# Kernel tuning notes

Measured on AMD Instinct MI355X. Metric: run time of the kernel, lower is better.

Reference implementation:

```python
import jax, jax.numpy as jnp
import numpy as np

B, S, D, H = 4, 2048, 1024, 16
HD = D // H  # head dim = 64


def setup_inputs() -> dict:
    key = jax.random.key(0)
    ks = jax.random.split(key, 6)
    scale = D ** -0.5
    x = jax.random.normal(ks[0], (B, S, D), dtype=jnp.float32)
    # per-head q/k/v projections stacked: [H, D, HD] (bias-free, as in GPT Head)
    Wq = jax.random.normal(ks[1], (H, D, HD), dtype=jnp.float32) * scale
    Wk = jax.random.normal(ks[2], (H, D, HD), dtype=jnp.float32) * scale
    Wv = jax.random.normal(ks[3], (H, D, HD), dtype=jnp.float32) * scale
    # output projection Linear(D, D) with bias
    Wp = jax.random.normal(ks[4], (D, D), dtype=jnp.float32) * scale
    bp = jax.random.normal(ks[5], (D,), dtype=jnp.float32) * 0.01
    return {"x": x, "Wq": Wq, "Wk": Wk, "Wv": Wv, "Wp": Wp, "bp": bp}


def reference(x, Wq, Wk, Wv, Wp, bp):
    # q,k,v: [B, H, S, HD]
    q = jnp.einsum("bsd,hdk->bhsk", x, Wq)
    k = jnp.einsum("bsd,hdk->bhsk", x, Wk)
    v = jnp.einsum("bsd,hdk->bhsk", x, Wv)
    scale = HD ** -0.5
    # attention scores [B, H, S, S] with causal mask
    scores = jnp.einsum("bhsk,bhtk->bhst", q, k) * scale
    causal = jnp.tril(jnp.ones((S, S), dtype=bool))
    scores = jnp.where(causal, scores, jnp.finfo(scores.dtype).min)
    att = jax.nn.softmax(scores, axis=-1)
    out = jnp.einsum("bhst,bhtk->bhsk", att, v)  # [B, H, S, HD]
    # concat heads -> [B, S, D], then output projection
    out = out.transpose(0, 2, 1, 3).reshape(B, S, D)
    return out @ Wp + bp
```

## Files before the change

kernel.cpp:

```cpp
#include <hip/hip_runtime.h>
#include <stdint.h>

#define B_  4
#define S_  2048
#define D_  1024
#define H_  16
#define HD_ 64

typedef __attribute__((ext_vector_type(8))) short bf16x8;
typedef __attribute__((ext_vector_type(4))) short bf16x4;
typedef __attribute__((ext_vector_type(4))) float f32x4;

#define MFMA32(a, b, c) __builtin_amdgcn_mfma_f32_16x16x32_bf16(a, b, c, 0, 0, 0)

__device__ __forceinline__ unsigned short f2bf(float f) {
  union { float f; uint32_t u; } cv; cv.f = f;
  uint32_t x = cv.u;
  uint32_t r = (x + 0x7fffu + ((x >> 16) & 1u)) >> 16;
  return (unsigned short)r;
}

__device__ __forceinline__ unsigned short f2bf_rz(float f) {
  union { float f; uint32_t u; } cv; cv.f = f;
  return (unsigned short)(cv.u >> 16);
}

__device__ __forceinline__ float fexp2(float x) {
#if __has_builtin(__builtin_amdgcn_exp2f)
  return __builtin_amdgcn_exp2f(x);
#else
  return exp2f(x);
#endif
}

__device__ __forceinline__ void gload_lds16(const unsigned short* g, unsigned short* l) {
  __builtin_amdgcn_global_load_lds((const __attribute__((address_space(1))) void*)g,
                                   (__attribute__((address_space(3))) void*)l, 16, 0, 0);
}

__global__ void k_cast_x(const float* __restrict__ x, unsigned short* __restrict__ xb) {
  size_t i = ((size_t)blockIdx.x * 256 + threadIdx.x) * 8;
  float4 a = *(const float4*)(x + i);
  float4 b = *(const float4*)(x + i + 4);
  bf16x8 o;
  o[0] = (short)f2bf(a.x); o[1] = (short)f2bf(a.y);
  o[2] = (short)f2bf(a.z); o[3] = (short)f2bf(a.w);
  o[4] = (short)f2bf(b.x); o[5] = (short)f2bf(b.y);
  o[6] = (short)f2bf(b.z); o[7] = (short)f2bf(b.w);
  *(bf16x8*)(xb + i) = o;
}

__global__ void k_wqkv_t(const float* __restrict__ Wq, const float* __restrict__ Wk,
                         const float* __restrict__ Wv, unsigned short* __restrict__ W1T) {
  __shared__ unsigned short tile[64][65];
  const float* W = (blockIdx.z == 0) ? Wq : (blockIdx.z == 1) ? Wk : Wv;
  int h = blockIdx.y;
  int d0 = blockIdx.x * 64;
  int tx = threadIdx.x & 63;
  int tg = threadIdx.x >> 6;
  const float* src = W + (size_t)h * (D_ * HD_) + (size_t)d0 * HD_;
#pragma unroll
  for (int r = 0; r < 16; ++r) {
    int dy = tg * 16 + r;
    tile[tx][dy] = f2bf(src[(size_t)dy * HD_ + tx]);
  }
  __syncthreads();
  unsigned short* dst = W1T + ((size_t)blockIdx.z * 1024 + (size_t)h * 64) * 1024 + d0;
#pragma unroll
  for (int r = 0; r < 16; ++r) {
    int hd = tg * 16 + r;
    dst[(size_t)hd * 1024 + tx] = tile[hd][tx];
  }
}

__global__ void k_wp_t(const float* __restrict__ Wp, unsigned short* __restrict__ WpT) {
  __shared__ unsigned short tile[64][65];
  int n0 = blockIdx.x * 64, k0 = blockIdx.y * 64;
  int tx = threadIdx.x & 63;
  int tg = threadIdx.x >> 6;
#pragma unroll
  for (int r = 0; r < 16; ++r) {
    int ky = tg * 16 + r;
    tile[tx][ky] = f2bf(Wp[(size_t)(k0 + ky) * D_ + n0 + tx]);
  }
  __syncthreads();
#pragma unroll
  for (int r = 0; r < 16; ++r) {
    int ny = tg * 16 + r;
    WpT[(size_t)(n0 + ny) * D_ + k0 + tx] = tile[ny][tx];
  }
}

__device__ __forceinline__ void stage_half(const unsigned short* g0, unsigned short* l0, int tid) {
  int r0 = tid >> 2, s0 = tid & 3;
  gload_lds16(g0 + (size_t)r0 * 1024 + ((s0 ^ ((r0 >> 1) & 3)) << 3), l0 + tid * 8);
  int r1 = r0 + 128;
  gload_lds16(g0 + (size_t)r1 * 1024 + ((s0 ^ ((r1 >> 1) & 3)) << 3), l0 + 4096 + tid * 8);
}

__device__ __forceinline__ bf16x8 rd_swz(const unsigned short* base, int row, int g) {
  return *(const bf16x8*)&base[row * 32 + ((g ^ ((row >> 1) & 3)) << 3)];
}

__global__ __launch_bounds__(512, 2) void k_gemm_qk(const unsigned short* __restrict__ xb,
                                                    const unsigned short* __restrict__ W1T,
                                                    unsigned short* __restrict__ qb,
                                                    unsigned short* __restrict__ kb) {
  __shared__ __align__(16) unsigned short As[32768];
  __shared__ __align__(16) unsigned short Bs[32768];
  int tid = threadIdx.x;
  int lane = tid & 63;
  int wid = tid >> 6;
  int c = lane & 15, g = lane >> 4;
  int wr = wid >> 2, wc = wid & 3;
  int bid = blockIdx.x;
  int xcd = bid & 7, idx = bid >> 3;
  int by = (xcd << 2) | (idx & 3);
  int bx = idx >> 2;
  int m0 = by << 8, n0 = bx << 8;
  const unsigned short* gA = xb + (size_t)m0 * 1024;
  const unsigned short* gB = W1T + (size_t)n0 * 1024;

  f32x4 acc[8][4];
#pragma unroll
  for (int i = 0; i < 8; ++i)
#pragma unroll
    for (int n = 0; n < 4; ++n) acc[i][n] = (f32x4){0.f, 0.f, 0.f, 0.f};

  stage_half(gA + 0,  As + 0, tid);
  stage_half(gB + 0,  Bs + 0, tid);
  stage_half(gA + 32, As + 8192, tid);
  stage_half(gB + 32, Bs + 8192, tid);

  for (int t = 0; t < 16; ++t) {
    int sl = (t & 1) << 14;
    int so = sl ^ 16384;
    int kn = (t + 1) << 6;
    bool pf = (t < 15);
    const unsigned short* Asl = As + sl;
    const unsigned short* Bsl = Bs + sl;
    bf16x8 bf[4];

    asm volatile("s_waitcnt vmcnt(4)" ::: "memory");
    __builtin_amdgcn_s_barrier();
    if (pf) stage_half(gA + kn, As + so, tid);
#pragma unroll
    for (int n = 0; n < 4; ++n) bf[n] = rd_swz(Bsl, wc * 64 + n * 16 + c, g);
    {
      bf16x8 af[4];
#pragma unroll
      for (int j = 0; j < 4; ++j) af[j] = rd_swz(Asl, wr * 128 + j * 16 + c, g);
      __builtin_amdgcn_s_setprio(1);
#pragma unroll
      for (int j = 0; j < 4; ++j)
#pragma unroll
        for (int n = 0; n < 4; ++n) acc[j][n] = MFMA32(af[j], bf[n], acc[j][n]);
      __builtin_amdgcn_s_setprio(0);
    }
    if (pf) stage_half(gB + kn, Bs + so, tid);
    {
      bf16x8 af[4];
#pragma unroll
      for (int j = 0; j < 4; ++j) af[j] = rd_swz(Asl, wr * 128 + (4 + j) * 16 + c, g);
      __builtin_amdgcn_s_setprio(1);
#pragma unroll
      for (int j = 0; j < 4; ++j)
#pragma unroll
        for (int n = 0; n < 4; ++n) acc[4 + j][n] = MFMA32(af[j], bf[n], acc[4 + j][n]);
      __builtin_amdgcn_s_setprio(0);
    }
    asm volatile("s_waitcnt vmcnt(4)" ::: "memory");
    __builtin_amdgcn_s_barrier();
    if (pf) stage_half(gA + kn + 32, As + so + 8192, tid);
#pragma unroll
    for (int n = 0; n < 4; ++n) bf[n] = rd_swz(Bsl + 8192, wc * 64 + n * 16 + c, g);
    {
      bf16x8 af[4];
#pragma unroll
      for (int j = 0; j < 4; ++j) af[j] = rd_swz(Asl + 8192, wr * 128 + j * 16 + c, g);
      __builtin_amdgcn_s_setprio(1);
#pragma unroll
      for (int j = 0; j < 4; ++j)
#pragma unroll
        for (int n = 0; n < 4; ++n) acc[j][n] = MFMA32(af[j], bf[n], acc[j][n]);
      __builtin_amdgcn_s_setprio(0);
    }
    if (pf) stage_half(gB + kn + 32, Bs + so + 8192, tid);
    {
      bf16x8 af[4];
#pragma unroll
      for (int j = 0; j < 4; ++j) af[j] = rd_swz(Asl + 8192, wr * 128 + (4 + j) * 16 + c, g);
      __builtin_amdgcn_s_setprio(1);
#pragma unroll
      for (int j = 0; j < 4; ++j)
#pragma unroll
        for (int n = 0; n < 4; ++n) acc[4 + j][n] = MFMA32(af[j], bf[n], acc[4 + j][n]);
      __builtin_amdgcn_s_setprio(0);
    }
  }

  int Cnb = n0 + wc * 64;
  int qkv = Cnb >> 10;
  int h = (Cnb >> 6) & 15;
  int b = m0 >> 11;
  int s0 = m0 & 2047;
  unsigned short* dst = ((qkv == 0) ? qb : kb) + ((size_t)(b * 16 + h) * S_) * HD_;
  float sc = (qkv == 0) ? 0.18033688011112042f : 1.0f;
#pragma unroll
  for (int mrep = 0; mrep < 8; ++mrep)
#pragma unroll
    for (int n = 0; n < 4; ++n)
#pragma unroll
      for (int r = 0; r < 4; ++r) {
        int s = s0 + wr * 128 + mrep * 16 + 4 * g + r;
        int hd = n * 16 + c;
        dst[(size_t)s * HD_ + hd] = f2bf(acc[mrep][n][r] * sc);
      }
}

__global__ __launch_bounds__(256) void k_gemm_vt(const unsigned short* __restrict__ W1T,
                                                 const unsigned short* __restrict__ xb,
                                                 unsigned short* __restrict__ vt) {
  __shared__ __align__(16) unsigned short As[128 * 32];
  __shared__ __align__(16) unsigned short Bs[128 * 32];
  const int K = 1024;
  int tid = threadIdx.x;
  int lane = tid & 63;
  int w = tid >> 6;
  int c = lane & 15, g = lane >> 4;
  int wr = w >> 1, wc = w & 1;
  int nwg = gridDim.x * gridDim.y;
  int bid = blockIdx.y * gridDim.x + blockIdx.x;
  int swzb = (bid & 7) * (nwg >> 3) + (bid >> 3);
  int bx = swzb % gridDim.x, by = swzb / gridDim.x;
  int m0 = by * 128;
  int n0 = bx * 128;
  const unsigned short* Av = W1T + (size_t)2048 * 1024;
  f32x4 acc[4][4];
#pragma unroll
  for (int m = 0; m < 4; ++m)
#pragma unroll
    for (int n = 0; n < 4; ++n) acc[m][n] = (f32x4){0.f, 0.f, 0.f, 0.f};

  int t0 = tid, t1 = tid + 256;
  const unsigned short* ga0 = Av + (size_t)(m0 + (t0 >> 2)) * K + 8 * (t0 & 3);
  const unsigned short* ga1 = Av + (size_t)(m0 + (t1 >> 2)) * K + 8 * (t1 & 3);
  const unsigned short* gb0 = xb + (size_t)(n0 + (t0 >> 2)) * K + 8 * (t0 & 3);
  const unsigned short* gb1 = xb + (size_t)(n0 + (t1 >> 2)) * K + 8 * (t1 & 3);

  for (int kk = 0; kk < K; kk += 32) {
    __syncthreads();
    gload_lds16(ga0 + kk, &As[t0 * 8]);
    gload_lds16(ga1 + kk, &As[t1 * 8]);
    gload_lds16(gb0 + kk, &Bs[t0 * 8]);
    gload_lds16(gb1 + kk, &Bs[t1 * 8]);
    __syncthreads();
    bf16x8 af[4], bfr[4];
#pragma unroll
    for (int m = 0; m < 4; ++m)
      af[m] = *(const bf16x8*)&As[(wr * 64 + m * 16 + c) * 32 + 8 * g];
#pragma unroll
    for (int n = 0; n < 4; ++n)
      bfr[n] = *(const bf16x8*)&Bs[(wc * 64 + n * 16 + c) * 32 + 8 * g];
#pragma unroll
    for (int m = 0; m < 4; ++m)
#pragma unroll
      for (int n = 0; n < 4; ++n) acc[m][n] = MFMA32(af[m], bfr[n], acc[m][n]);
  }

  int b = (n0 >> 11);
#pragma unroll
  for (int m = 0; m < 4; ++m)
#pragma unroll
    for (int n = 0; n < 4; ++n)
#pragma unroll
      for (int r = 0; r < 4; ++r) {
        int vm = m0 + wr * 64 + m * 16 + 4 * g + r;
        int Cn = n0 + wc * 64 + n * 16 + c;
        int s = Cn & 2047;
        vt[((size_t)(b << 10) + vm) * S_ + s] = f2bf(acc[m][n][r]);
      }
}

__device__ __forceinline__ void stage_kv(const unsigned short* kp, const unsigned short* vp,
                                         int tb, unsigned short* Ks, unsigned short* Vs,
                                         int tid) {
  int i0 = tid, i1 = tid + 256;
  int r0 = i0 >> 3, ch0 = ((i0 & 7) ^ (r0 & 7)) << 3;
  int r1 = i1 >> 3, ch1 = ((i1 & 7) ^ (r1 & 7)) << 3;
  gload_lds16(kp + (size_t)(tb + r0) * HD_ + ch0, &Ks[i0 * 8]);
  gload_lds16(kp + (size_t)(tb + r1) * HD_ + ch1, &Ks[i1 * 8]);
  gload_lds16(vp + (size_t)r0 * S_ + tb + ch0, &Vs[i0 * 8]);
  gload_lds16(vp + (size_t)r1 * S_ + tb + ch1, &Vs[i1 * 8]);
}

__global__ __launch_bounds__(256) void k_attn(const unsigned short* __restrict__ qb,
                                              const unsigned short* __restrict__ kb,
                                              const unsigned short* __restrict__ vt,
                                              unsigned short* __restrict__ attn) {
  __shared__ __align__(16) unsigned short Ks[2][64 * 64];
  __shared__ __align__(16) unsigned short Vs[2][64 * 64];
  int tid = threadIdx.x;
  int lane = tid & 63;
  int w = tid >> 6;
  int c = lane & 15, g = lane >> 4;
  int bid = blockIdx.x;
  int xcd = bid & 7, idx = bid >> 3;
  int bh = (xcd << 3) | (idx & 7);
  int j = 15 - (idx >> 3);
  const unsigned short* kp = kb + (size_t)bh * S_ * HD_;
  const unsigned short* vp = vt + (size_t)bh * HD_ * S_;
  int b = bh >> 4, h = bh & 15;

  int q0w = j * 128 + w * 32;
  const unsigned short* qp = qb + ((size_t)bh * S_ + q0w) * HD_;
  bf16x8 qf[2][2];
#pragma unroll
  for (int qs = 0; qs < 2; ++qs)
#pragma unroll
    for (int h2 = 0; h2 < 2; ++h2)
      qf[qs][h2] = *(const bf16x8*)(qp + (size_t)(qs * 16 + c) * HD_ + h2 * 32 + 8 * g);

  const f32x4 fz = {0.f, 0.f, 0.f, 0.f};
  f32x4 oacc[4][2];
#pragma unroll
  for (int c4 = 0; c4 < 4; ++c4)
#pragma unroll
    for (int qs = 0; qs < 2; ++qs) oacc[c4][qs] = fz;
  float m[2] = {-1e30f, -1e30f};
  float l[2] = {0.f, 0.f};

  int nkb = 2 * j + 2;
  int nkw = (q0w + 95) >> 6;

  stage_kv(kp, vp, 0, Ks[0], Vs[0], tid);
  __syncthreads();

  for (int kt = 0; kt < nkb; ++kt) {
    int cur = kt & 1;
    if (kt + 1 < nkb) stage_kv(kp, vp, (kt + 1) << 6, Ks[cur ^ 1], Vs[cur ^ 1], tid);
    if (kt < nkw) {
      int tb = kt << 6;
      const unsigned short* KsC = Ks[cur];
      const unsigned short* VsC = Vs[cur];
      f32x4 st[4][2];
#pragma unroll
      for (int k4 = 0; k4 < 4; ++k4) {
        int row = k4 * 16 + c;
        int rx = row & 7;
        bf16x8 a0 = *(const bf16x8*)&KsC[row * 64 + ((g ^ rx) << 3)];
        bf16x8 a1 = *(const bf16x8*)&KsC[row * 64 + (((4 + g) ^ rx) << 3)];
#pragma unroll
        for (int qs = 0; qs < 2; ++qs) {
          f32x4 t0 = MFMA32(a0, qf[qs][0], fz);
          st[k4][qs] = MFMA32(a1, qf[qs][1], t0);
        }
      }
      if (tb + 63 > q0w) {
#pragma unroll
        for (int k4 = 0; k4 < 4; ++k4)
#pragma unroll
          for (int qs = 0; qs < 2; ++qs)
#pragma unroll
            for (int r = 0; r < 4; ++r)
              if (tb + k4 * 16 + 4 * g + r > q0w + qs * 16 + c) st[k4][qs][r] = -1e30f;
      }
      bf16x8 pa[2][2];
#pragma unroll
      for (int qs = 0; qs < 2; ++qs) {
        float mx = -1e30f;
#pragma unroll
        for (int k4 = 0; k4 < 4; ++k4)
#pragma unroll
          for (int r = 0; r < 4; ++r) mx = fmaxf(mx, st[k4][qs][r]);
        mx = fmaxf(mx, __shfl_xor(mx, 16));
        mx = fmaxf(mx, __shfl_xor(mx, 32));
        if (!__all(mx - m[qs] <= 8.f)) {
          float m_new = fmaxf(m[qs], mx);
          float resc = fexp2(m[qs] - m_new);
          m[qs] = m_new;
          float rb0 = __shfl(resc, 4 * g + 0);
          float rb1 = __shfl(resc, 4 * g + 1);
          float rb2 = __shfl(resc, 4 * g + 2);
          float rb3 = __shfl(resc, 4 * g + 3);
#pragma unroll
          for (int c4 = 0; c4 < 4; ++c4) {
            oacc[c4][qs][0] *= rb0; oacc[c4][qs][1] *= rb1;
            oacc[c4][qs][2] *= rb2; oacc[c4][qs][3] *= rb3;
          }
          l[qs] *= resc;
        }
        float mh = m[qs];
        float rs = 0.f;
#pragma unroll
        for (int k4 = 0; k4 < 4; ++k4)
#pragma unroll
          for (int r = 0; r < 4; ++r) {
            float e = fexp2(st[k4][qs][r] - mh);
            st[k4][qs][r] = e;
            rs += e;
          }
        rs += __shfl_xor(rs, 16);
        rs += __shfl_xor(rs, 32);
        l[qs] += rs;
#pragma unroll
        for (int ks = 0; ks < 2; ++ks)
#pragma unroll
          for (int jj = 0; jj < 8; ++jj)
            pa[qs][ks][jj] = (short)f2bf_rz(st[ks * 2 + (jj >> 2)][qs][jj & 3]);
      }
#pragma unroll
      for (int c4 = 0; c4 < 4; ++c4) {
        int row = c4 * 16 + c;
        int rx = row & 7;
#pragma unroll
        for (int ks = 0; ks < 2; ++ks) {
          int e0 = ks * 32 + 4 * g;
          int e1 = e0 + 16;
          int s0 = (((e0 >> 3) ^ rx) << 3) | (e0 & 7);
          int s1 = (((e1 >> 3) ^ rx) << 3) | (e1 & 7);
          bf16x4 v0 = *(const bf16x4*)&VsC[row * 64 + s0];
          bf16x4 v1 = *(const bf16x4*)&VsC[row * 64 + s1];
          bf16x8 vf;
          vf[0] = v0[0]; vf[1] = v0[1]; vf[2] = v0[2]; vf[3] = v0[3];
          vf[4] = v1[0]; vf[5] = v1[1]; vf[6] = v1[2]; vf[7] = v1[3];
#pragma unroll
          for (int qs = 0; qs < 2; ++qs)
            oacc[c4][qs] = MFMA32(pa[qs][ks], vf, oacc[c4][qs]);
        }
      }
    }
    __syncthreads();
  }
#pragma unroll
  for (int qs = 0; qs < 2; ++qs) {
    float linv = 1.f / l[qs];
    float lb0 = __shfl(linv, 4 * g + 0);
    float lb1 = __shfl(linv, 4 * g + 1);
    float lb2 = __shfl(linv, 4 * g + 2);
    float lb3 = __shfl(linv, 4 * g + 3);
    float lb[4] = {lb0, lb1, lb2, lb3};
    unsigned short* op = attn + ((size_t)b * S_ + q0w + qs * 16) * D_ + h * HD_;
#pragma unroll
    for (int c4 = 0; c4 < 4; ++c4)
#pragma unroll
      for (int r = 0; r < 4; ++r)
        op[(size_t)(4 * g + r) * D_ + c4 * 16 + c] = f2bf(oacc[c4][qs][r] * lb[r]);
  }
}

__global__ __launch_bounds__(256) void k_gemm_out(const unsigned short* __restrict__ at,
                                                  const unsigned short* __restrict__ WpT,
                                                  const float* __restrict__ bp,
                                                  float* __restrict__ out) {
  __shared__ __align__(16) unsigned short As[128 * 32];
  __shared__ __align__(16) unsigned short Bs[128 * 32];
  const int K = 1024;
  int tid = threadIdx.x;
  int lane = tid & 63;
  int w = tid >> 6;
  int c = lane & 15, g = lane >> 4;
  int wr = w >> 1, wc = w & 1;
  int nwg = gridDim.x * gridDim.y;
  int bid = blockIdx.y * gridDim.x + blockIdx.x;
  int swzb = (bid & 7) * (nwg >> 3) + (bid >> 3);
  int bx = swzb % gridDim.x, by = swzb / gridDim.x;
  int m0 = by * 128;
  int n0 = bx * 128;
  f32x4 acc[4][4];
#pragma unroll
  for (int m = 0; m < 4; ++m)
#pragma unroll
    for (int n = 0; n < 4; ++n) acc[m][n] = (f32x4){0.f, 0.f, 0.f, 0.f};

  int t0 = tid, t1 = tid + 256;
  const unsigned short* ga0 = at + (size_t)(m0 + (t0 >> 2)) * K + 8 * (t0 & 3);
  const unsigned short* ga1 = at + (size_t)(m0 + (t1 >> 2)) * K + 8 * (t1 & 3);
  const unsigned short* gb0 = WpT + (size_t)(n0 + (t0 >> 2)) * K + 8 * (t0 & 3);
  const unsigned short* gb1 = WpT + (size_t)(n0 + (t1 >> 2)) * K + 8 * (t1 & 3);

  for (int kk = 0; kk < K; kk += 32) {
    __syncthreads();
    gload_lds16(ga0 + kk, &As[t0 * 8]);
    gload_lds16(ga1 + kk, &As[t1 * 8]);
    gload_lds16(gb0 + kk, &Bs[t0 * 8]);
    gload_lds16(gb1 + kk, &Bs[t1 * 8]);
    __syncthreads();
    bf16x8 af[4], bfr[4];
#pragma unroll
    for (int m = 0; m < 4; ++m)
      af[m] = *(const bf16x8*)&As[(wr * 64 + m * 16 + c) * 32 + 8 * g];
#pragma unroll
    for (int n = 0; n < 4; ++n)
      bfr[n] = *(const bf16x8*)&Bs[(wc * 64 + n * 16 + c) * 32 + 8 * g];
#pragma unroll
    for (int m = 0; m < 4; ++m)
#pragma unroll
      for (int n = 0; n < 4; ++n) acc[m][n] = MFMA32(af[m], bfr[n], acc[m][n]);
  }

#pragma unroll
  for (int m = 0; m < 4; ++m)
#pragma unroll
    for (int n = 0; n < 4; ++n)
#pragma unroll
      for (int r = 0; r < 4; ++r) {
        int R = m0 + wr * 64 + m * 16 + 4 * g + r;
        int Cn = n0 + wc * 64 + n * 16 + c;
        out[(size_t)R * D_ + Cn] = acc[m][n][r] + bp[Cn];
      }
}

extern "C" void kernel_launch(void* const* d_in, const int* in_sizes, int n_in,
                              void* d_out, int out_size, void* d_ws, size_t ws_size,
                              hipStream_t stream) {
  const float* x  = (const float*)d_in[0];
  const float* Wq = (const float*)d_in[1];
  const float* Wk = (const float*)d_in[2];
  const float* Wv = (const float*)d_in[3];
  const float* Wp = (const float*)d_in[4];
  const float* bp = (const float*)d_in[5];
  float* out = (float*)d_out;
  char* ws = (char*)d_ws;
  unsigned short* xb  = (unsigned short*)(ws);
  unsigned short* w1t = (unsigned short*)(ws + (size_t)(16u << 20));
  unsigned short* wpt = (unsigned short*)(ws + (size_t)(22u << 20));
  unsigned short* qb  = (unsigned short*)(ws + (size_t)(24u << 20));
  unsigned short* kb  = (unsigned short*)(ws + (size_t)(40u << 20));
  unsigned short* vt  = (unsigned short*)(ws + (size_t)(56u << 20));
  unsigned short* at  = xb;

  k_cast_x<<<dim3(4096), dim3(256), 0, stream>>>(x, xb);
  k_wqkv_t<<<dim3(16, 16, 3), dim3(256), 0, stream>>>(Wq, Wk, Wv, w1t);
  k_wp_t<<<dim3(16, 16), dim3(256), 0, stream>>>(Wp, wpt);
  k_gemm_qk<<<dim3(256), dim3(512), 0, stream>>>(xb, w1t, qb, kb);
  k_gemm_vt<<<dim3(64, 8), dim3(256), 0, stream>>>(w1t, xb, vt);
  k_attn<<<dim3(1024), dim3(256), 0, stream>>>(qb, kb, vt, at);
  k_gemm_out<<<dim3(8, 64), dim3(256), 0, stream>>>(at, wpt, bp, out);
}
```

Baseline: 180.8 us.

## Pipeline V and output GEMMs with double-buffered swizzled LDS and larger tiles

Rewrites the V-projection and output-projection GEMMs to use 512-thread blocks with 128x256 and 256x128 tiles. They stage data through double-buffered, XOR-swizzled LDS with async global-to-LDS loads that overlap the MFMA work, following the QK GEMM design. The attention kernel now precomputes its swizzled LDS offsets outside the loop and packs P to bf16 with a byte-permute. The final pipeline iteration also drains outstanding loads with vmcnt(0). This adds LDS use and register pressure and relies on careful waitcnt accounting.

```diff
diff --git a/kernel.cpp b/kernel.cpp
--- a/kernel.cpp
+++ b/kernel.cpp
@@ -20,16 +20,21 @@
   return (unsigned short)r;
 }
 
-__device__ __forceinline__ unsigned short f2bf_rz(float f) {
-  union { float f; uint32_t u; } cv; cv.f = f;
-  return (unsigned short)(cv.u >> 16);
-}
-
 __device__ __forceinline__ float fexp2(float x) {
 #if __has_builtin(__builtin_amdgcn_exp2f)
   return __builtin_amdgcn_exp2f(x);
 #else
   return exp2f(x);
+#endif
+}
+
+__device__ __forceinline__ uint32_t pk2(float lo, float hi) {
+  union { float f; uint32_t u; } a, b;
+  a.f = lo; b.f = hi;
+#if __has_builtin(__builtin_amdgcn_perm)
+  return __builtin_amdgcn_perm(b.u, a.u, 0x07060302u);
+#else
+  return (b.u & 0xffff0000u) | (a.u >> 16);
 #endif
 }
 
@@ -96,6 +101,10 @@
   gload_lds16(g0 + (size_t)r0 * 1024 + ((s0 ^ ((r0 >> 1) & 3)) << 3), l0 + tid * 8);
   int r1 = r0 + 128;
   gload_lds16(g0 + (size_t)r1 * 1024 + ((s0 ^ ((r1 >> 1) & 3)) << 3), l0 + 4096 + tid * 8);
+}
+__device__ __forceinline__ void stage_rows128(const unsigned short* g0, unsigned short* l0, int tid) {
+  int r0 = tid >> 2, s0 = tid & 3;
+  gload_lds16(g0 + (size_t)r0 * 1024 + ((s0 ^ ((r0 >> 1) & 3)) << 3), l0 + tid * 8);
 }
 
 __device__ __forceinline__ bf16x8 rd_swz(const unsigned short* base, int row, int g) {
@@ -169,7 +178,8 @@
         for (int n = 0; n < 4; ++n) acc[4 + j][n] = MFMA32(af[j], bf[n], acc[4 + j][n]);
       __builtin_amdgcn_s_setprio(0);
     }
-    asm volatile("s_waitcnt vmcnt(4)" ::: "memory");
+    if (pf) asm volatile("s_waitcnt vmcnt(4)" ::: "memory");
+    else    asm volatile("s_waitcnt vmcnt(0)" ::: "memory");
     __builtin_amdgcn_s_barrier();
     if (pf) stage_half(gA + kn + 32, As + so + 8192, tid);
 #pragma unroll
@@ -218,67 +228,222 @@
       }
 }
 
-__global__ __launch_bounds__(256) void k_gemm_vt(const unsigned short* __restrict__ W1T,
-                                                 const unsigned short* __restrict__ xb,
-                                                 unsigned short* __restrict__ vt) {
-  __shared__ __align__(16) unsigned short As[128 * 32];
-  __shared__ __align__(16) unsigned short Bs[128 * 32];
-  const int K = 1024;
+__global__ __launch_bounds__(512, 2) void k_gemm_vt(const unsigned short* __restrict__ W1T,
+                                                    const unsigned short* __restrict__ xb,
+                                                    unsigned short* __restrict__ vt) {
+  __shared__ __align__(16) unsigned short As[16384];
+  __shared__ __align__(16) unsigned short Bs[32768];
   int tid = threadIdx.x;
   int lane = tid & 63;
-  int w = tid >> 6;
+  int wid = tid >> 6;
   int c = lane & 15, g = lane >> 4;
-  int wr = w >> 1, wc = w & 1;
-  int nwg = gridDim.x * gridDim.y;
-  int bid = blockIdx.y * gridDim.x + blockIdx.x;
-  int swzb = (bid & 7) * (nwg >> 3) + (bid >> 3);
-  int bx = swzb % gridDim.x, by = swzb / gridDim.x;
-  int m0 = by * 128;
-  int n0 = bx * 128;
-  const unsigned short* Av = W1T + (size_t)2048 * 1024;
+  int wr = wid >> 2, wc = wid & 3;
+  int bid = blockIdx.x;
+  int by = bid & 7;
+  int bx = bid >> 3;
+  int m0 = by << 7, n0 = bx << 8;
+  const unsigned short* gA = W1T + (size_t)(2048 + m0) * 1024;
+  const unsigned short* gB = xb + (size_t)n0 * 1024;
+
   f32x4 acc[4][4];
 #pragma unroll
   for (int m = 0; m < 4; ++m)
 #pragma unroll
     for (int n = 0; n < 4; ++n) acc[m][n] = (f32x4){0.f, 0.f, 0.f, 0.f};
 
-  int t0 = tid, t1 = tid + 256;
-  const unsigned short* ga0 = Av + (size_t)(m0 + (t0 >> 2)) * K + 8 * (t0 & 3);
-  const unsigned short* ga1 = Av + (size_t)(m0 + (t1 >> 2)) * K + 8 * (t1 & 3);
-  const unsigned short* gb0 = xb + (size_t)(n0 + (t0 >> 2)) * K + 8 * (t0 & 3);
-  const unsigned short* gb1 = xb + (size_t)(n0 + (t1 >> 2)) * K + 8 * (t1 & 3);
-
-  for (int kk = 0; kk < K; kk += 32) {
-    __syncthreads();
-    gload_lds16(ga0 + kk, &As[t0 * 8]);
-    gload_lds16(ga1 + kk, &As[t1 * 8]);
-    gload_lds16(gb0 + kk, &Bs[t0 * 8]);
-    gload_lds16(gb1 + kk, &Bs[t1 * 8]);
-    __syncthreads();
-    bf16x8 af[4], bfr[4];
-#pragma unroll
-    for (int m = 0; m < 4; ++m)
-      af[m] = *(const bf16x8*)&As[(wr * 64 + m * 16 + c) * 32 + 8 * g];
+  stage_rows128(gA + 0,  As + 0, tid);
+  stage_half  (gB + 0,  Bs + 0, tid);
+  stage_rows128(gA + 32, As + 4096, tid);
+  stage_half  (gB + 32, Bs + 8192, tid);
+
+  for (int t = 0; t < 16; ++t) {
+    int slA = (t & 1) << 13, soA = slA ^ 8192;
+    int slB = (t & 1) << 14, soB = slB ^ 16384;
+    int kn = (t + 1) << 6;
+    bool pf = (t < 15);
+    const unsigned short* Asl = As + slA;
+    const unsigned short* Bsl = Bs + slB;
+    bf16x8 af[4];
+
+    asm volatile("s_waitcnt vmcnt(3)" ::: "memory");
+    __builtin_amdgcn_s_barrier();
+    if (pf) stage_rows128(gA + kn, As + soA, tid);
+#pragma unroll
+    for (int j = 0; j < 4; ++j) af[j] = rd_swz(Asl, wr * 64 + j * 16 + c, g);
+    {
+      bf16x8 bf[2];
+#pragma unroll
+      for (int n = 0; n < 2; ++n) bf[n] = rd_swz(Bsl, wc * 64 + n * 16 + c, g);
+      __builtin_amdgcn_s_setprio(1);
+#pragma unroll
+      for (int j = 0; j < 4; ++j)
+#pragma unroll
+        for (int n = 0; n < 2; ++n) acc[j][n] = MFMA32(af[j], bf[n], acc[j][n]);
+      __builtin_amdgcn_s_setprio(0);
+    }
+    if (pf) stage_half(gB + kn, Bs + soB, tid);
+    {
+      bf16x8 bf[2];
+#pragma unroll
+      for (int n = 0; n < 2; ++n) bf[n] = rd_swz(Bsl, wc * 64 + (2 + n) * 16 + c, g);
+      __builtin_amdgcn_s_setprio(1);
+#pragma unroll
+      for (int j = 0; j < 4; ++j)
+#pragma unroll
+        for (int n = 0; n < 2; ++n) acc[j][2 + n] = MFMA32(af[j], bf[n], acc[j][2 + n]);
+      __builtin_amdgcn_s_setprio(0);
+    }
+    if (pf) asm volatile("s_waitcnt vmcnt(3)" ::: "memory");
+    else    asm volatile("s_waitcnt vmcnt(0)" ::: "memory");
+    __builtin_amdgcn_s_barrier();
+    if (pf) stage_rows128(gA + kn + 32, As + soA + 4096, tid);
+#pragma unroll
+    for (int j = 0; j < 4; ++j) af[j] = rd_swz(Asl + 4096, wr * 64 + j * 16 + c, g);
+    {
+      bf16x8 bf[2];
+#pragma unroll
+      for (int n = 0; n < 2; ++n) bf[n] = rd_swz(Bsl + 8192, wc * 64 + n * 16 + c, g);
+      __builtin_amdgcn_s_setprio(1);
+#pragma unroll
+      for (int j = 0; j < 4; ++j)
+#pragma unroll
+        for (int n = 0; n < 2; ++n) acc[j][n] = MFMA32(af[j], bf[n], acc[j][n]);
+      __builtin_amdgcn_s_setprio(0);
+    }
+    if (pf) stage_half(gB + kn + 32, Bs + soB + 8192, tid);
+    {
+      bf16x8 bf[2];
+#pragma unroll
+      for (int n = 0; n < 2; ++n) bf[n] = rd_swz(Bsl + 8192, wc * 64 + (2 + n) * 16 + c, g);
+      __builtin_amdgcn_s_setprio(1);
+#pragma unroll
+      for (int j = 0; j < 4; ++j)
+#pragma unroll
+        for (int n = 0; n < 2; ++n) acc[j][2 + n] = MFMA32(af[j], bf[n], acc[j][2 + n]);
+      __builtin_amdgcn_s_setprio(0);
+    }
+  }
+
+#pragma unroll
+  for (int m = 0; m < 4; ++m)
 #pragma unroll
     for (int n = 0; n < 4; ++n)
-      bfr[n] = *(const bf16x8*)&Bs[(wc * 64 + n * 16 + c) * 32 + 8 * g];
-#pragma unroll
-    for (int m = 0; m < 4; ++m)
-#pragma unroll
-      for (int n = 0; n < 4; ++n) acc[m][n] = MFMA32(af[m], bfr[n], acc[m][n]);
-  }
-
-  int b = (n0 >> 11);
-#pragma unroll
-  for (int m = 0; m < 4; ++m)
-#pragma unroll
-    for (int n = 0; n < 4; ++n)
 #pragma unroll
       for (int r = 0; r < 4; ++r) {
-        int vm = m0 + wr * 64 + m * 16 + 4 * g + r;
-        int Cn = n0 + wc * 64 + n * 16 + c;
-        int s = Cn & 2047;
-        vt[((size_t)(b << 10) + vm) * S_ + s] = f2bf(acc[m][n][r]);
+        int vrow = m0 + wr * 64 + m * 16 + 4 * g + r;
+        int N = n0 + wc * 64 + n * 16 + c;
+        int b = N >> 11, s = N & 2047;
+        vt[((size_t)(b << 10) + vrow) * S_ + s] = f2bf(acc[m][n][r]);
+      }
+}
+
+__global__ __launch_bounds__(512, 2) void k_gemm_out(const unsigned short* __restrict__ at,
+                                                     const unsigned short* __restrict__ WpT,
+                                                     const float* __restrict__ bp,
+                                                     float* __restrict__ out) {
+  __shared__ __align__(16) unsigned short As[32768];
+  __shared__ __align__(16) unsigned short Bs[16384];
+  int tid = threadIdx.x;
+  int lane = tid & 63;
+  int wid = tid >> 6;
+  int c = lane & 15, g = lane >> 4;
+  int wr = wid >> 2, wc = wid & 3;
+  int bid = blockIdx.x;
+  int xcd = bid & 7, idx = bid >> 3;
+  int by = (xcd << 2) | (idx & 3);
+  int bx = idx >> 2;
+  int m0 = by << 8, n0 = bx << 7;
+  const unsigned short* gA = at + (size_t)m0 * 1024;
+  const unsigned short* gB = WpT + (size_t)n0 * 1024;
+
+  f32x4 acc[8][2];
+#pragma unroll
+  for (int i = 0; i < 8; ++i)
+#pragma unroll
+    for (int n = 0; n < 2; ++n) acc[i][n] = (f32x4){0.f, 0.f, 0.f, 0.f};
+
+  stage_half   (gA + 0,  As + 0, tid);
+  stage_rows128(gB + 0,  Bs + 0, tid);
+  stage_half   (gA + 32, As + 8192, tid);
+  stage_rows128(gB + 32, Bs + 4096, tid);
+
+  for (int t = 0; t < 16; ++t) {
+    int slA = (t & 1) << 14, soA = slA ^ 16384;
+    int slB = (t & 1) << 13, soB = slB ^ 8192;
+    int kn = (t + 1) << 6;
+    bool pf = (t < 15);
+    const unsigned short* Asl = As + slA;
+    const unsigned short* Bsl = Bs + slB;
+    bf16x8 bf[2];
+
+    asm volatile("s_waitcnt vmcnt(3)" ::: "memory");
+    __builtin_amdgcn_s_barrier();
+    if (pf) stage_half(gA + kn, As + soA, tid);
+#pragma unroll
+    for (int n = 0; n < 2; ++n) bf[n] = rd_swz(Bsl, wc * 32 + n * 16 + c, g);
+    {
+      bf16x8 af[4];
+#pragma unroll
+      for (int j = 0; j < 4; ++j) af[j] = rd_swz(Asl, wr * 128 + j * 16 + c, g);
+      __builtin_amdgcn_s_setprio(1);
+#pragma unroll
+      for (int j = 0; j < 4; ++j)
+#pragma unroll
+        for (int n = 0; n < 2; ++n) acc[j][n] = MFMA32(af[j], bf[n], acc[j][n]);
+      __builtin_amdgcn_s_setprio(0);
+    }
+    if (pf) stage_rows128(gB + kn, Bs + soB, tid);
+    {
+      bf16x8 af[4];
+#pragma unroll
+      for (int j = 0; j < 4; ++j) af[j] = rd_swz(Asl, wr * 128 + (4 + j) * 16 + c, g);
+      __builtin_amdgcn_s_setprio(1);
+#pragma unroll
+      for (int j = 0; j < 4; ++j)
+#pragma unroll
+        for (int n = 0; n < 2; ++n) acc[4 + j][n] = MFMA32(af[j], bf[n], acc[4 + j][n]);
+      __builtin_amdgcn_s_setprio(0);
+    }
+    if (pf) asm volatile("s_waitcnt vmcnt(3)" ::: "memory");
+    else    asm volatile("s_waitcnt vmcnt(0)" ::: "memory");
+    __builtin_amdgcn_s_barrier();
+    if (pf) stage_half(gA + kn + 32, As + soA + 8192, tid);
+#pragma unroll
+    for (int n = 0; n < 2; ++n) bf[n] = rd_swz(Bsl + 4096, wc * 32 + n * 16 + c, g);
+    {
+      bf16x8 af[4];
+#pragma unroll
+      for (int j = 0; j < 4; ++j) af[j] = rd_swz(Asl + 8192, wr * 128 + j * 16 + c, g);
+      __builtin_amdgcn_s_setprio(1);
+#pragma unroll
+      for (int j = 0; j < 4; ++j)
+#pragma unroll
+        for (int n = 0; n < 2; ++n) acc[j][n] = MFMA32(af[j], bf[n], acc[j][n]);
+      __builtin_amdgcn_s_setprio(0);
+    }
+    if (pf) stage_rows128(gB + kn + 32, Bs + soB + 4096, tid);
+    {
+      bf16x8 af[4];
+#pragma unroll
+      for (int j = 0; j < 4; ++j) af[j] = rd_swz(Asl + 8192, wr * 128 + (4 + j) * 16 + c, g);
+      __builtin_amdgcn_s_setprio(1);
+#pragma unroll
+      for (int j = 0; j < 4; ++j)
+#pragma unroll
+        for (int n = 0; n < 2; ++n) acc[4 + j][n] = MFMA32(af[j], bf[n], acc[4 + j][n]);
+      __builtin_amdgcn_s_setprio(0);
+    }
+  }
+
+#pragma unroll
+  for (int mrep = 0; mrep < 8; ++mrep)
+#pragma unroll
+    for (int n = 0; n < 2; ++n)
+#pragma unroll
+      for (int r = 0; r < 4; ++r) {
+        int R = m0 + wr * 128 + mrep * 16 + 4 * g + r;
+        int Cn = n0 + wc * 32 + n * 16 + c;
+        out[(size_t)R * D_ + Cn] = acc[mrep][n][r] + bp[Cn];
       }
 }
 
@@ -312,6 +477,25 @@
   const unsigned short* vp = vt + (size_t)bh * HD_ * S_;
   int b = bh >> 4, h = bh & 15;
 
+  int koff[4][2], voff[4][2][2];
+#pragma unroll
+  for (int k4 = 0; k4 < 4; ++k4) {
+    int row = k4 * 16 + c, rx = row & 7;
+    koff[k4][0] = row * 64 + ((g ^ rx) << 3);
+    koff[k4][1] = row * 64 + (((4 + g) ^ rx) << 3);
+  }
+#pragma unroll
+  for (int c4 = 0; c4 < 4; ++c4) {
+    int row = c4 * 16 + c, rx = row & 7;
+#pragma unroll
+    for (int ks = 0; ks < 2; ++ks) {
+      int e0 = ks * 32 + 4 * g;
+      int e1 = e0 + 16;
+      voff[c4][ks][0] = row * 64 + ((((e0 >> 3) ^ rx) << 3) | (e0 & 7));
+      voff[c4][ks][1] = row * 64 + ((((e1 >> 3) ^ rx) << 3) | (e1 & 7));
+    }
+  }
+
   int q0w = j * 128 + w * 32;
   const unsigned short* qp = qb + ((size_t)bh * S_ + q0w) * HD_;
   bf16x8 qf[2][2];
@@ -346,10 +530,8 @@
       f32x4 st[4][2];
 #pragma unroll
       for (int k4 = 0; k4 < 4; ++k4) {
-        int row = k4 * 16 + c;
-        int rx = row & 7;
-        bf16x8 a0 = *(const bf16x8*)&KsC[row * 64 + ((g ^ rx) << 3)];
-        bf16x8 a1 = *(const bf16x8*)&KsC[row * 64 + (((4 + g) ^ rx) << 3)];
+        bf16x8 a0 = *(const bf16x8*)&KsC[koff[k4][0]];
+        bf16x8 a1 = *(const bf16x8*)&KsC[koff[k4][1]];
 #pragma unroll
         for (int qs = 0; qs < 2; ++qs) {
           f32x4 t0 = MFMA32(a0, qf[qs][0], fz);
@@ -404,23 +586,22 @@
         rs += __shfl_xor(rs, 32);
         l[qs] += rs;
 #pragma unroll
-        for (int ks = 0; ks < 2; ++ks)
-#pragma unroll
-          for (int jj = 0; jj < 8; ++jj)
-            pa[qs][ks][jj] = (short)f2bf_rz(st[ks * 2 + (jj >> 2)][qs][jj & 3]);
+        for (int ks = 0; ks < 2; ++ks) {
+          union { uint32_t wd[4]; bf16x8 v; } pu;
+          int ks2 = ks * 2;
+          pu.wd[0] = pk2(st[ks2][qs][0], st[ks2][qs][1]);
+          pu.wd[1] = pk2(st[ks2][qs][2], st[ks2][qs][3]);
+          pu.wd[2] = pk2(st[ks2 + 1][qs][0], st[ks2 + 1][qs][1]);
+          pu.wd[3] = pk2(st[ks2 + 1][qs][2], st[ks2 + 1][qs][3]);
+          pa[qs][ks] = pu.v;
+        }
       }
 #pragma unroll
       for (int c4 = 0; c4 < 4; ++c4) {
-        int row = c4 * 16 + c;
-        int rx = row & 7;
 #pragma unroll
         for (int ks = 0; ks < 2; ++ks) {
-          int e0 = ks * 32 + 4 * g;
-          int e1 = e0 + 16;
-          int s0 = (((e0 >> 3) ^ rx) << 3) | (e0 & 7);
-          int s1 = (((e1 >> 3) ^ rx) << 3) | (e1 & 7);
-          bf16x4 v0 = *(const bf16x4*)&VsC[row * 64 + s0];
-          bf16x4 v1 = *(const bf16x4*)&VsC[row * 64 + s1];
+          bf16x4 v0 = *(const bf16x4*)&VsC[voff[c4][ks][0]];
+          bf16x4 v1 = *(const bf16x4*)&VsC[voff[c4][ks][1]];
           bf16x8 vf;
           vf[0] = v0[0]; vf[1] = v0[1]; vf[2] = v0[2]; vf[3] = v0[3];
           vf[4] = v1[0]; vf[5] = v1[1]; vf[6] = v1[2]; vf[7] = v1[3];
@@ -447,68 +628,6 @@
       for (int r = 0; r < 4; ++r)
         op[(size_t)(4 * g + r) * D_ + c4 * 16 + c] = f2bf(oacc[c4][qs][r] * lb[r]);
   }
-}
-
-__global__ __launch_bounds__(256) void k_gemm_out(const unsigned short* __restrict__ at,
-                                                  const unsigned short* __restrict__ WpT,
-                                                  const float* __restrict__ bp,
-                                                  float* __restrict__ out) {
-  __shared__ __align__(16) unsigned short As[128 * 32];
-  __shared__ __align__(16) unsigned short Bs[128 * 32];
-  const int K = 1024;
-  int tid = threadIdx.x;
-  int lane = tid & 63;
-  int w = tid >> 6;
-  int c = lane & 15, g = lane >> 4;
-  int wr = w >> 1, wc = w & 1;
-  int nwg = gridDim.x * gridDim.y;
-  int bid = blockIdx.y * gridDim.x + blockIdx.x;
-  int swzb = (bid & 7) * (nwg >> 3) + (bid >> 3);
-  int bx = swzb % gridDim.x, by = swzb / gridDim.x;
-  int m0 = by * 128;
-  int n0 = bx * 128;
-  f32x4 acc[4][4];
-#pragma unroll
-  for (int m = 0; m < 4; ++m)
-#pragma unroll
-    for (int n = 0; n < 4; ++n) acc[m][n] = (f32x4){0.f, 0.f, 0.f, 0.f};
-
-  int t0 = tid, t1 = tid + 256;
-  const unsigned short* ga0 = at + (size_t)(m0 + (t0 >> 2)) * K + 8 * (t0 & 3);
-  const unsigned short* ga1 = at + (size_t)(m0 + (t1 >> 2)) * K + 8 * (t1 & 3);
-  const unsigned short* gb0 = WpT + (size_t)(n0 + (t0 >> 2)) * K + 8 * (t0 & 3);
-  const unsigned short* gb1 = WpT + (size_t)(n0 + (t1 >> 2)) * K + 8 * (t1 & 3);
-
-  for (int kk = 0; kk < K; kk += 32) {
-    __syncthreads();
-    gload_lds16(ga0 + kk, &As[t0 * 8]);
-    gload_lds16(ga1 + kk, &As[t1 * 8]);
-    gload_lds16(gb0 + kk, &Bs[t0 * 8]);
-    gload_lds16(gb1 + kk, &Bs[t1 * 8]);
-    __syncthreads();
-    bf16x8 af[4], bfr[4];
-#pragma unroll
-    for (int m = 0; m < 4; ++m)
-      af[m] = *(const bf16x8*)&As[(wr * 64 + m * 16 + c) * 32 + 8 * g];
-#pragma unroll
-    for (int n = 0; n < 4; ++n)
-      bfr[n] = *(const bf16x8*)&Bs[(wc * 64 + n * 16 + c) * 32 + 8 * g];
-#pragma unroll
-    for (int m = 0; m < 4; ++m)
-#pragma unroll
-      for (int n = 0; n < 4; ++n) acc[m][n] = MFMA32(af[m], bfr[n], acc[m][n]);
-  }
-
-#pragma unroll
-  for (int m = 0; m < 4; ++m)
-#pragma unroll
-    for (int n = 0; n < 4; ++n)
-#pragma unroll
-      for (int r = 0; r < 4; ++r) {
-        int R = m0 + wr * 64 + m * 16 + 4 * g + r;
-        int Cn = n0 + wc * 64 + n * 16 + c;
-        out[(size_t)R * D_ + Cn] = acc[m][n][r] + bp[Cn];
-      }
 }
 
 extern "C" void kernel_launch(void* const* d_in, const int* in_sizes, int n_in,
@@ -534,7 +653,7 @@
   k_wqkv_t<<<dim3(16, 16, 3), dim3(256), 0, stream>>>(Wq, Wk, Wv, w1t);
   k_wp_t<<<dim3(16, 16), dim3(256), 0, stream>>>(Wp, wpt);
   k_gemm_qk<<<dim3(256), dim3(512), 0, stream>>>(xb, w1t, qb, kb);
-  k_gemm_vt<<<dim3(64, 8), dim3(256), 0, stream>>>(w1t, xb, vt);
+  k_gemm_vt<<<dim3(256), dim3(512), 0, stream>>>(w1t, xb, vt);
   k_attn<<<dim3(1024), dim3(256), 0, stream>>>(qb, kb, vt, at);
-  k_gemm_out<<<dim3(8, 64), dim3(256), 0, stream>>>(at, wpt, bp, out);
-}
+  k_gemm_out<<<dim3(256), dim3(512), 0, stream>>>(at, wpt, bp, out);
+}
```

Result: slower. 194.0 us (+7.3%).
